# Optimization experiments

Measured on AMD Instinct MI355X. Metric: run time of the kernel, lower is better.

Reference implementation:

```python
import jax, jax.numpy as jnp
import numpy as np

B, T, H, L, OUT = 64, 2048, 256, 2, 256


def setup_inputs() -> dict:
    key = jax.random.key(0)
    ks = jax.random.split(key, 7)
    s = 1.0 / np.sqrt(H)
    return {
        "x": jax.random.normal(ks[0], (B, T, H), dtype=jnp.float32),
        "W_ih": jax.random.uniform(ks[1], (L, 4 * H, H), jnp.float32, -s, s),
        "W_hh": jax.random.uniform(ks[2], (L, 4 * H, H), jnp.float32, -s, s),
        "b_ih": jax.random.uniform(ks[3], (L, 4 * H), jnp.float32, -s, s),
        "b_hh": jax.random.uniform(ks[4], (L, 4 * H), jnp.float32, -s, s),
        "W_fc": jax.random.uniform(ks[5], (OUT, H), jnp.float32, -s, s),
        "b_fc": jax.random.uniform(ks[6], (OUT,), jnp.float32, -s, s),
    }


def _lstm_forward(x, W_ih, W_hh, b_ih, b_hh, W_fc, b_fc):
    n_layers = W_ih.shape[0]
    batch = x.shape[0]
    hidden = W_hh.shape[2]
    h0 = jnp.zeros((n_layers, batch, hidden), x.dtype)
    c0 = jnp.zeros((n_layers, batch, hidden), x.dtype)

    def step(carry, x_t):
        h, c = carry  # [L, B, H] each
        inp = x_t  # [B, in]
        new_h, new_c = [], []
        for l in range(n_layers):
            # gates: [B, 4H] = x W_ih^T + b_ih + h W_hh^T + b_hh
            gates = (inp @ W_ih[l].T + b_ih[l]) + (h[l] @ W_hh[l].T + b_hh[l])
            i_g, f_g, g_g, o_g = jnp.split(gates, 4, axis=-1)
            c_new = jax.nn.sigmoid(f_g) * c[l] + jax.nn.sigmoid(i_g) * jnp.tanh(g_g)
            h_new = jax.nn.sigmoid(o_g) * jnp.tanh(c_new)
            new_h.append(h_new)
            new_c.append(c_new)
            inp = h_new
        return (jnp.stack(new_h), jnp.stack(new_c)), None

    (h_T, _), _ = jax.lax.scan(step, (h0, c0), jnp.swapaxes(x, 0, 1))
    # fc applied to last timestep's top-layer hidden state
    return h_T[-1] @ W_fc.T + b_fc  # [B, OUT]


def reference(x, W_ih, W_hh, b_ih, b_hh, W_fc, b_fc):
    return _lstm_forward(x, W_ih, W_hh, b_ih, b_hh, W_fc, b_fc)
```

## Files before the change

kernel.cpp:

```cpp
#include <hip/hip_runtime.h>
#include <math.h>

typedef unsigned long long u64;
typedef __attribute__((ext_vector_type(8))) short short8v;
typedef __attribute__((ext_vector_type(4))) float f32x4;
typedef __attribute__((ext_vector_type(4))) unsigned uint4v;

#define LB 64
#define LT 2048
#define LH 256
#define LOUT 256
#define NWG 256

#define WS_CNT    0
#define WS_CNT_SZ (12 * 1024)
#define TICK_OFF  2048
#define WS_H1     (64 * 1024)
#define WS_H2     (WS_H1 + 256 * 1024)
#define WS_BIAS   (WS_H2 + 256 * 1024)
#define WS_WT2    (1024 * 1024)

#define MFMA(a, b, c) __builtin_amdgcn_mfma_f32_16x16x32_bf16(a, b, c, 0, 0, 0)

__device__ __host__ __forceinline__ short bf16_rne(float f) {
    unsigned u = __builtin_bit_cast(unsigned, f);
    unsigned r = (u + 0x7fffu + ((u >> 16) & 1u)) >> 16;
    return (short)r;
}
__device__ __forceinline__ float bf16_to_f(short s) {
    unsigned u = ((unsigned)(unsigned short)s) << 16;
    return __builtin_bit_cast(float, u);
}
__device__ __forceinline__ float fsigm(float g) {
    return __builtin_amdgcn_rcpf(1.f + __builtin_amdgcn_exp2f(g * -1.44269504f));
}
__device__ __forceinline__ float ftanh(float g) {
    return __builtin_amdgcn_rcpf(1.f + __builtin_amdgcn_exp2f(g * -2.88539008f)) * 2.f - 1.f;
}

template <int LOCAL>
__device__ __forceinline__ int ld_flag(const int* p) {
    int v; u64 a = (u64)p;
    if (LOCAL) asm volatile("global_load_dword %0, %1, off sc0\n\ts_waitcnt vmcnt(0)"
                            : "=&v"(v) : "v"(a) : "memory");
    else       asm volatile("global_load_dword %0, %1, off sc0 sc1\n\ts_waitcnt vmcnt(0)"
                            : "=&v"(v) : "v"(a) : "memory");
    return v;
}
template <int LOCAL>
__device__ __forceinline__ void st_flag(int* p, int v) {
    u64 a = (u64)p;
    if (LOCAL) asm volatile("global_store_dword %0, %1, off sc0" :: "v"(a), "v"(v) : "memory");
    else       asm volatile("global_store_dword %0, %1, off sc0 sc1" :: "v"(a), "v"(v) : "memory");
}
template <int LOCAL>
__device__ __forceinline__ void st_unit(void* p, uint4v d) {
    u64 a = (u64)p;
    if (LOCAL) asm volatile("global_store_dwordx4 %0, %1, off sc0" :: "v"(a), "v"(d) : "memory");
    else       asm volatile("global_store_dwordx4 %0, %1, off sc0 sc1" :: "v"(a), "v"(d) : "memory");
}
template <int LOCAL>
__device__ __forceinline__ void ld_units(u64 a0, u64 a1, u64 a2, u64 a3,
        uint4v& U0, uint4v& U1, uint4v& U2, uint4v& U3,
        uint4v& U4, uint4v& U5, uint4v& U6, uint4v& U7) {
    if (LOCAL) asm volatile(
        "global_load_dwordx4 %0, %8, off sc0\n\t"
        "global_load_dwordx4 %1, %8, off offset:16 sc0\n\t"
        "global_load_dwordx4 %2, %9, off sc0\n\t"
        "global_load_dwordx4 %3, %9, off offset:16 sc0\n\t"
        "global_load_dwordx4 %4, %10, off sc0\n\t"
        "global_load_dwordx4 %5, %10, off offset:16 sc0\n\t"
        "global_load_dwordx4 %6, %11, off sc0\n\t"
        "global_load_dwordx4 %7, %11, off offset:16 sc0\n\t"
        "s_waitcnt vmcnt(0)"
        : "=&v"(U0), "=&v"(U1), "=&v"(U2), "=&v"(U3),
          "=&v"(U4), "=&v"(U5), "=&v"(U6), "=&v"(U7)
        : "v"(a0), "v"(a1), "v"(a2), "v"(a3) : "memory");
    else asm volatile(
        "global_load_dwordx4 %0, %8, off sc0 sc1\n\t"
        "global_load_dwordx4 %1, %8, off offset:16 sc0 sc1\n\t"
        "global_load_dwordx4 %2, %9, off sc0 sc1\n\t"
        "global_load_dwordx4 %3, %9, off offset:16 sc0 sc1\n\t"
        "global_load_dwordx4 %4, %10, off sc0 sc1\n\t"
        "global_load_dwordx4 %5, %10, off offset:16 sc0 sc1\n\t"
        "global_load_dwordx4 %6, %11, off sc0 sc1\n\t"
        "global_load_dwordx4 %7, %11, off offset:16 sc0 sc1\n\t"
        "s_waitcnt vmcnt(0)"
        : "=&v"(U0), "=&v"(U1), "=&v"(U2), "=&v"(U3),
          "=&v"(U4), "=&v"(U5), "=&v"(U6), "=&v"(U7)
        : "v"(a0), "v"(a1), "v"(a2), "v"(a3) : "memory");
}

__global__ void prep_weights(const float* __restrict__ W_ih,
                             const float* __restrict__ W_hh,
                             const float* __restrict__ b_ih,
                             const float* __restrict__ b_hh,
                             unsigned short* __restrict__ Wt2,
                             float* __restrict__ bias_r) {
    int gid = blockIdx.x * 256 + threadIdx.x;
    if (gid >= (1 << 20)) return;
    int j   = gid & 7;
    int rwi = (gid >> 3) & 15;
    int kgi = (gid >> 7) & 3;
    int ks  = (gid >> 9) & 15;
    int mt  = (gid >> 13) & 3;
    int s   = (gid >> 15) & 15;
    int layer = gid >> 19;
    int k   = ks * 32 + kgi * 8 + j;
    int row = mt * 256 + s * 16 + rwi;
    float w = (k < 256) ? W_ih[((size_t)layer * 1024 + row) * 256 + k]
                        : W_hh[((size_t)layer * 1024 + row) * 256 + (k - 256)];
    short hi = bf16_rne(w);
    float rem = w - bf16_to_f(hi);
    short lo = bf16_rne(rem);
    size_t base = (((size_t)((layer * 16 + s) * 4 + mt) * 16 + ks) * 1024)
                  + (size_t)kgi * 128 + rwi * 8 + j;
    Wt2[base]       = (unsigned short)hi;
    Wt2[base + 512] = (unsigned short)lo;
    if (k == 0) {
        int ridx = s * 64 + mt * 16 + rwi;
        bias_r[layer * 1024 + ridx] = b_ih[layer * 1024 + row] + b_hh[layer * 1024 + row];
    }
}

__global__ __launch_bounds__(256, 1)
void lstm_persistent(const float* __restrict__ x,
                     const unsigned short* __restrict__ Wt2,
                     const float* __restrict__ bias_r,
                     char* __restrict__ h1c, char* __restrict__ h2c,
                     int* __restrict__ cnt)
{
    __shared__ __align__(16) f32x4 red[12][64];
    __shared__ int s_mode, s_bg, s_role;

    const int tid   = threadIdx.x;
    const int wave  = tid >> 6;
    const int lane  = tid & 63;

    if (tid == 0) {
        unsigned xcc = (unsigned)__builtin_amdgcn_s_getreg(20 | (3 << 11)) & 7u;
        int* tick = cnt + TICK_OFF;
        int tk = __hip_atomic_fetch_add(tick + xcc, 1, __ATOMIC_RELAXED, __HIP_MEMORY_SCOPE_AGENT);
        __hip_atomic_fetch_add(tick + 8, 1, __ATOMIC_RELEASE, __HIP_MEMORY_SCOPE_AGENT);
        while (__hip_atomic_load(tick + 8, __ATOMIC_ACQUIRE, __HIP_MEMORY_SCOPE_AGENT) < NWG)
            __builtin_amdgcn_s_sleep(8);
        int bal = 1;
        for (int i = 0; i < 8; ++i)
            bal &= (__hip_atomic_load(tick + i, __ATOMIC_RELAXED, __HIP_MEMORY_SCOPE_AGENT) == 32);
        s_mode = bal;
        s_bg   = bal ? (int)xcc : (int)(blockIdx.x & 7);
        s_role = bal ? tk : (int)(((blockIdx.x >> 7) << 4) | ((blockIdx.x & 127) >> 3));
    }
    __syncthreads();

    __builtin_amdgcn_fence(__ATOMIC_SEQ_CST, "agent");
    __syncthreads();
    if (tid == 0) {
        int* b2 = cnt + TICK_OFF + 16;
        __hip_atomic_fetch_add(b2, 1, __ATOMIC_RELEASE, __HIP_MEMORY_SCOPE_AGENT);
        while (__hip_atomic_load(b2, __ATOMIC_ACQUIRE, __HIP_MEMORY_SCOPE_AGENT) < NWG)
            __builtin_amdgcn_s_sleep(8);
    }
    __syncthreads();

    const int mode  = s_mode;
    const int bg    = s_bg;
    const int layer = s_role >> 4;
    const int s     = s_role & 15;
    const int b0    = bg * 8;
    const int kg    = lane >> 4;
    const int rw    = lane & 15;
    const int rb    = rw & 7;
    const int batch = b0 + rb;
    int* const fl_base = cnt + bg * 256;

    short8v Ahi[4][4], Alo[4][4];
    #pragma unroll
    for (int mt = 0; mt < 4; ++mt)
        #pragma unroll
        for (int k2 = 0; k2 < 4; ++k2) {
            size_t base = (((size_t)((layer * 16 + s) * 4 + mt) * 16 + (wave * 4 + k2)) * 1024)
                          + (size_t)kg * 128 + rw * 8;
            Ahi[mt][k2] = *(const short8v*)((const short*)Wt2 + base);
            Alo[mt][k2] = *(const short8v*)((const short*)Wt2 + base + 512);
        }

    f32x4 biasv[4];
    #pragma unroll
    for (int mt = 0; mt < 4; ++mt)
        biasv[mt] = *(const f32x4*)(bias_r + layer * 1024 + s * 64 + mt * 16 + kg * 4);

    f32x4 creg = {0.f, 0.f, 0.f, 0.f};

    float4 xr[4][2];
    if (layer == 0 && wave < 2) {
        #pragma unroll
        for (int k2 = 0; k2 < 4; ++k2) {
            const int kbase = (wave * 4 + k2) * 32 + kg * 8;
            const float* xp = x + ((size_t)batch * LT + 0) * LH + kbase;
            xr[k2][0] = *(const float4*)xp;
            xr[k2][1] = *(const float4*)(xp + 4);
        }
    }

    for (int r = 0; r <= LT; ++r) {
        const bool active = (layer == 0) ? (r < LT) : (r >= 1);
        const int t = (layer == 0) ? r : (r - 1);

        short8v Bhi[4], Blo[4];
        bool useB = false;
        if (active) {
            if (layer == 0 && wave < 2) {
                #pragma unroll
                for (int k2 = 0; k2 < 4; ++k2) {
                    float fv[8] = {xr[k2][0].x, xr[k2][0].y, xr[k2][0].z, xr[k2][0].w,
                                   xr[k2][1].x, xr[k2][1].y, xr[k2][1].z, xr[k2][1].w};
                    short8v bh, bl;
                    #pragma unroll
                    for (int j = 0; j < 8; ++j) {
                        short hb = bf16_rne(fv[j]);
                        bh[j] = hb;
                        bl[j] = bf16_rne(fv[j] - bf16_to_f(hb));
                    }
                    Bhi[k2] = bh; Blo[k2] = bl;
                }
                useB = true;
            } else {
                const char* hbuf; int slot, kofs; bool any;
                if (layer == 0)      { any = (t > 0); hbuf = h1c; slot = (t - 1) & 3; kofs = -256; }
                else if (wave < 2)   { any = true;    hbuf = h1c; slot = t & 3;       kofs = 0;    }
                else                 { any = (t > 0); hbuf = h2c; slot = (t - 1) & 3; kofs = -256; }
                if (any) {
                    const int kb0 = wave * 128 + kg * 8 + kofs;
                    u64 a0, a1, a2, a3;
                    {
                        int kb;
                        kb = kb0;       a0 = (u64)(hbuf + (size_t)((((slot * 64 + batch) * 16) + (kb >> 4)) * 4 + ((kb >> 2) & 3)) * 16);
                        kb = kb0 + 32;  a1 = (u64)(hbuf + (size_t)((((slot * 64 + batch) * 16) + (kb >> 4)) * 4 + ((kb >> 2) & 3)) * 16);
                        kb = kb0 + 64;  a2 = (u64)(hbuf + (size_t)((((slot * 64 + batch) * 16) + (kb >> 4)) * 4 + ((kb >> 2) & 3)) * 16);
                        kb = kb0 + 96;  a3 = (u64)(hbuf + (size_t)((((slot * 64 + batch) * 16) + (kb >> 4)) * 4 + ((kb >> 2) & 3)) * 16);
                    }
                    uint4v U0, U1, U2, U3, U4, U5, U6, U7;
                    if (mode) ld_units<1>(a0, a1, a2, a3, U0, U1, U2, U3, U4, U5, U6, U7);
                    else      ld_units<0>(a0, a1, a2, a3, U0, U1, U2, U3, U4, U5, U6, U7);
                    union { unsigned d[4]; short8v v; } bh, bl;
                    bh.d[0] = U0.x; bh.d[1] = U0.y; bh.d[2] = U1.x; bh.d[3] = U1.y; Bhi[0] = bh.v;
                    bl.d[0] = U0.z; bl.d[1] = U0.w; bl.d[2] = U1.z; bl.d[3] = U1.w; Blo[0] = bl.v;
                    bh.d[0] = U2.x; bh.d[1] = U2.y; bh.d[2] = U3.x; bh.d[3] = U3.y; Bhi[1] = bh.v;
                    bl.d[0] = U2.z; bl.d[1] = U2.w; bl.d[2] = U3.z; bl.d[3] = U3.w; Blo[1] = bl.v;
                    bh.d[0] = U4.x; bh.d[1] = U4.y; bh.d[2] = U5.x; bh.d[3] = U5.y; Bhi[2] = bh.v;
                    bl.d[0] = U4.z; bl.d[1] = U4.w; bl.d[2] = U5.z; bl.d[3] = U5.w; Blo[2] = bl.v;
                    bh.d[0] = U6.x; bh.d[1] = U6.y; bh.d[2] = U7.x; bh.d[3] = U7.y; Bhi[3] = bh.v;
                    bl.d[0] = U6.z; bl.d[1] = U6.w; bl.d[2] = U7.z; bl.d[3] = U7.w; Blo[3] = bl.v;
                    useB = true;
                }
            }
        }

        f32x4 acc[4];
        #pragma unroll
        for (int mt = 0; mt < 4; ++mt) acc[mt] = (f32x4){0.f, 0.f, 0.f, 0.f};
        if (useB) {
            #pragma unroll
            for (int k2 = 0; k2 < 4; ++k2)
                #pragma unroll
                for (int mt = 0; mt < 4; ++mt) {
                    acc[mt] = MFMA(Ahi[mt][k2], Bhi[k2], acc[mt]);
                    acc[mt] = MFMA(Ahi[mt][k2], Blo[k2], acc[mt]);
                    acc[mt] = MFMA(Alo[mt][k2], Bhi[k2], acc[mt]);
                }
        }

        if (active && wave > 0) {
            #pragma unroll
            for (int mt = 0; mt < 4; ++mt) red[(wave - 1) * 4 + mt][lane] = acc[mt];
        }
        __syncthreads();

        if (active && wave == 0) {
            f32x4 gate[4];
            #pragma unroll
            for (int mt = 0; mt < 4; ++mt) {
                f32x4 gs = acc[mt] + biasv[mt];
                #pragma unroll
                for (int w = 0; w < 3; ++w) gs += red[w * 4 + mt][lane];
                gate[mt] = gs;
            }
            float hv[4];
            #pragma unroll
            for (int rr = 0; rr < 4; ++rr) {
                float si = fsigm(gate[0][rr]);
                float sf = fsigm(gate[1][rr]);
                float so = fsigm(gate[3][rr]);
                float gg = ftanh(gate[2][rr]);
                float cn = sf * creg[rr] + si * gg;
                creg[rr] = cn;
                hv[rr] = so * ftanh(cn);
            }
            if (rw < 8) {
                u64 qh = 0, ql = 0;
                #pragma unroll
                for (int rr = 0; rr < 4; ++rr) {
                    unsigned short hb = (unsigned short)bf16_rne(hv[rr]);
                    unsigned short lb = (unsigned short)bf16_rne(hv[rr] - bf16_to_f((short)hb));
                    qh |= ((u64)hb) << (16 * rr);
                    ql |= ((u64)lb) << (16 * rr);
                }
                uint4v dd;
                dd.x = (unsigned)qh; dd.y = (unsigned)(qh >> 32);
                dd.z = (unsigned)ql; dd.w = (unsigned)(ql >> 32);
                char* hbuf = (layer == 0 ? h1c : h2c);
                int unit = (((t & 3) * 64 + (b0 + rw)) * 16 + s) * 4 + kg;
                if (mode) st_unit<1>(hbuf + (size_t)unit * 16, dd);
                else      st_unit<0>(hbuf + (size_t)unit * 16, dd);
            }
        }

        if (wave == 0 && r < LT) {
            asm volatile("s_waitcnt vmcnt(0)" ::: "memory");
            if (lane == 0) {
                int* fp = fl_base + (layer * 16 + s) * 16;
                if (mode) { st_flag<1>(fp, r + 1); st_flag<0>(fp, r + 1); }
                else      st_flag<0>(fp, r + 1);
            }
        }

        if (layer == 0 && wave < 2 && t + 1 < LT) {
            #pragma unroll
            for (int k2 = 0; k2 < 4; ++k2) {
                const int kbase = (wave * 4 + k2) * 32 + kg * 8;
                const float* xp = x + ((size_t)batch * LT + (t + 1)) * LH + kbase;
                xr[k2][0] = *(const float4*)xp;
                xr[k2][1] = *(const float4*)(xp + 4);
            }
        }

        if (r < LT) {
            if (wave == 0) {
                const int mL  = lane >> 4;
                const int tgt = (layer == 0) ? ((mL == 0) ? r + 1 : r - 1) : (r + 1);
                int* fp = fl_base + (lane & 31) * 16;
                int it = 0;
                for (;;) {
                    int v = 0x7fffffff;
                    if (lane < 32) {
                        ++it;
                        if (mode && (it & 7) != 0) v = ld_flag<1>(fp);
                        else                       v = ld_flag<0>(fp);
                    }
                    if (__all(v >= tgt)) break;
                    if (!mode) __builtin_amdgcn_s_sleep(1);
                }
            }
            __syncthreads();
        }
    }
}

__global__ __launch_bounds__(256)
void fc_kernel(const char* __restrict__ h2c,
               const float* __restrict__ W_fc,
               const float* __restrict__ b_fc,
               float* __restrict__ out) {
    int b = blockIdx.x;
    int o = threadIdx.x;
    __shared__ float hrow[LH];
    for (int k = threadIdx.x; k < LH; k += 256) {
        int unit = ((3 * 64 + b) * 16 + (k >> 4)) * 4 + ((k >> 2) & 3);
        const u64* up = (const u64*)(h2c + (size_t)unit * 16);
        u64 qh = up[0];
        u64 ql = up[1];
        int sh = (k & 3) * 16;
        hrow[k] = bf16_to_f((short)(qh >> sh)) + bf16_to_f((short)(ql >> sh));
    }
    __syncthreads();
    float acc = b_fc[o];
#pragma unroll 8
    for (int k = 0; k < LH; ++k)
        acc = fmaf(W_fc[o * LH + k], hrow[k], acc);
    out[b * LOUT + o] = acc;
}

extern "C" void kernel_launch(void* const* d_in, const int* in_sizes, int n_in,
                              void* d_out, int out_size, void* d_ws, size_t ws_size,
                              hipStream_t stream) {
    const float* x    = (const float*)d_in[0];
    const float* W_ih = (const float*)d_in[1];
    const float* W_hh = (const float*)d_in[2];
    const float* b_ih = (const float*)d_in[3];
    const float* b_hh = (const float*)d_in[4];
    const float* W_fc = (const float*)d_in[5];
    const float* b_fc = (const float*)d_in[6];
    float* out = (float*)d_out;

    char* ws = (char*)d_ws;
    int*            cnt    = (int*)(ws + WS_CNT);
    char*           h1c    = ws + WS_H1;
    char*           h2c    = ws + WS_H2;
    float*          bias_r = (float*)(ws + WS_BIAS);
    unsigned short* Wt2    = (unsigned short*)(ws + WS_WT2);

    hipMemsetAsync(cnt, 0, WS_CNT_SZ, stream);
    prep_weights<<<(1 << 20) / 256, 256, 0, stream>>>(W_ih, W_hh, b_ih, b_hh, Wt2, bias_r);

    void* args[] = {(void*)&x, (void*)&Wt2, (void*)&bias_r,
                    (void*)&h1c, (void*)&h2c, (void*)&cnt};
    hipError_t e = hipLaunchCooperativeKernel(lstm_persistent, dim3(NWG), dim3(256),
                                              args, 0, stream);
    if (e != hipSuccess) {
        lstm_persistent<<<NWG, 256, 0, stream>>>(x, Wt2, bias_r, h1c, h2c, cnt);
    }

    fc_kernel<<<LB, 256, 0, stream>>>(h2c, W_fc, b_fc, out);
}
```

Before: 8.370 ms.

## Distribute LSTM gate epilogue across all four waves with per-wave dword stores

Instead of wave 0 reducing partial gate sums from the other three waves and computing all four batch-row cell updates, every wave now writes its partials to shared memory and computes one cell element (selected by wave index), storing a packed hi/lo bf16 dword. The hidden-state layout changes from hi/lo 64-bit halves to interleaved hi/lo per element, so the consumer unpack and the fc kernel are adjusted to match. The x prefetch is moved before the MFMA section, and the flag publish moves after a new barrier, dropping the duplicate local store and polling the slower coherent path less often. This aims to shorten the serial epilogue on the critical path of each timestep, at the cost of an extra __syncthreads and four times as many narrower global stores per unit.

```diff
diff --git a/kernel.cpp b/kernel.cpp
--- a/kernel.cpp
+++ b/kernel.cpp
@@ -54,10 +54,10 @@
     else       asm volatile("global_store_dword %0, %1, off sc0 sc1" :: "v"(a), "v"(v) : "memory");
 }
 template <int LOCAL>
-__device__ __forceinline__ void st_unit(void* p, uint4v d) {
+__device__ __forceinline__ void st_dw(void* p, unsigned d) {
     u64 a = (u64)p;
-    if (LOCAL) asm volatile("global_store_dwordx4 %0, %1, off sc0" :: "v"(a), "v"(d) : "memory");
-    else       asm volatile("global_store_dwordx4 %0, %1, off sc0 sc1" :: "v"(a), "v"(d) : "memory");
+    if (LOCAL) asm volatile("global_store_dword %0, %1, off sc0" :: "v"(a), "v"(d) : "memory");
+    else       asm volatile("global_store_dword %0, %1, off sc0 sc1" :: "v"(a), "v"(d) : "memory");
 }
 template <int LOCAL>
 __device__ __forceinline__ void ld_units(u64 a0, u64 a1, u64 a2, u64 a3,
@@ -91,6 +91,21 @@
         : "v"(a0), "v"(a1), "v"(a2), "v"(a3) : "memory");
 }
 
+__device__ __forceinline__ void unpack_frag(const uint4v& Ua, const uint4v& Ub,
+                                            short8v& bh, short8v& bl) {
+    union { unsigned d[4]; short8v v; } H, L;
+    H.d[0] = (Ua.x & 0xffffu) | (Ua.y << 16);
+    H.d[1] = (Ua.z & 0xffffu) | (Ua.w << 16);
+    H.d[2] = (Ub.x & 0xffffu) | (Ub.y << 16);
+    H.d[3] = (Ub.z & 0xffffu) | (Ub.w << 16);
+    L.d[0] = (Ua.x >> 16) | (Ua.y & 0xffff0000u);
+    L.d[1] = (Ua.z >> 16) | (Ua.w & 0xffff0000u);
+    L.d[2] = (Ub.x >> 16) | (Ub.w & 0xffff0000u & 0xffff0000u) ;
+    L.d[2] = (Ub.x >> 16) | (Ub.y & 0xffff0000u);
+    L.d[3] = (Ub.z >> 16) | (Ub.w & 0xffff0000u);
+    bh = H.v; bl = L.v;
+}
+
 __global__ void prep_weights(const float* __restrict__ W_ih,
                              const float* __restrict__ W_hh,
                              const float* __restrict__ b_ih,
@@ -130,7 +145,7 @@
                      char* __restrict__ h1c, char* __restrict__ h2c,
                      int* __restrict__ cnt)
 {
-    __shared__ __align__(16) f32x4 red[12][64];
+    __shared__ __align__(16) f32x4 red[16][64];
     __shared__ int s_mode, s_bg, s_role;
 
     const int tid   = threadIdx.x;
@@ -185,12 +200,12 @@
             Alo[mt][k2] = *(const short8v*)((const short*)Wt2 + base + 512);
         }
 
-    f32x4 biasv[4];
+    float bias_w[4];
     #pragma unroll
     for (int mt = 0; mt < 4; ++mt)
-        biasv[mt] = *(const f32x4*)(bias_r + layer * 1024 + s * 64 + mt * 16 + kg * 4);
-
-    f32x4 creg = {0.f, 0.f, 0.f, 0.f};
+        bias_w[mt] = bias_r[layer * 1024 + s * 64 + mt * 16 + kg * 4 + wave];
+
+    float creg = 0.f;
 
     float4 xr[4][2];
     if (layer == 0 && wave < 2) {
@@ -225,6 +240,15 @@
                     Bhi[k2] = bh; Blo[k2] = bl;
                 }
                 useB = true;
+                if (t + 1 < LT) {
+                    #pragma unroll
+                    for (int k2 = 0; k2 < 4; ++k2) {
+                        const int kbase = (wave * 4 + k2) * 32 + kg * 8;
+                        const float* xp = x + ((size_t)batch * LT + (t + 1)) * LH + kbase;
+                        xr[k2][0] = *(const float4*)xp;
+                        xr[k2][1] = *(const float4*)(xp + 4);
+                    }
+                }
             } else {
                 const char* hbuf; int slot, kofs; bool any;
                 if (layer == 0)      { any = (t > 0); hbuf = h1c; slot = (t - 1) & 3; kofs = -256; }
@@ -243,15 +267,10 @@
                     uint4v U0, U1, U2, U3, U4, U5, U6, U7;
                     if (mode) ld_units<1>(a0, a1, a2, a3, U0, U1, U2, U3, U4, U5, U6, U7);
                     else      ld_units<0>(a0, a1, a2, a3, U0, U1, U2, U3, U4, U5, U6, U7);
-                    union { unsigned d[4]; short8v v; } bh, bl;
-                    bh.d[0] = U0.x; bh.d[1] = U0.y; bh.d[2] = U1.x; bh.d[3] = U1.y; Bhi[0] = bh.v;
-                    bl.d[0] = U0.z; bl.d[1] = U0.w; bl.d[2] = U1.z; bl.d[3] = U1.w; Blo[0] = bl.v;
-                    bh.d[0] = U2.x; bh.d[1] = U2.y; bh.d[2] = U3.x; bh.d[3] = U3.y; Bhi[1] = bh.v;
-                    bl.d[0] = U2.z; bl.d[1] = U2.w; bl.d[2] = U3.z; bl.d[3] = U3.w; Blo[1] = bl.v;
-                    bh.d[0] = U4.x; bh.d[1] = U4.y; bh.d[2] = U5.x; bh.d[3] = U5.y; Bhi[2] = bh.v;
-                    bl.d[0] = U4.z; bl.d[1] = U4.w; bl.d[2] = U5.z; bl.d[3] = U5.w; Blo[2] = bl.v;
-                    bh.d[0] = U6.x; bh.d[1] = U6.y; bh.d[2] = U7.x; bh.d[3] = U7.y; Bhi[3] = bh.v;
-                    bl.d[0] = U6.z; bl.d[1] = U6.w; bl.d[2] = U7.z; bl.d[3] = U7.w; Blo[3] = bl.v;
+                    unpack_frag(U0, U1, Bhi[0], Blo[0]);
+                    unpack_frag(U2, U3, Bhi[1], Blo[1]);
+                    unpack_frag(U4, U5, Bhi[2], Blo[2]);
+                    unpack_frag(U6, U7, Bhi[3], Blo[3]);
                     useB = true;
                 }
             }
@@ -271,72 +290,50 @@
                 }
         }
 
-        if (active && wave > 0) {
+        if (active) {
             #pragma unroll
-            for (int mt = 0; mt < 4; ++mt) red[(wave - 1) * 4 + mt][lane] = acc[mt];
+            for (int mt = 0; mt < 4; ++mt) red[wave * 4 + mt][lane] = acc[mt];
         }
         __syncthreads();
 
-        if (active && wave == 0) {
-            f32x4 gate[4];
+        if (active) {
+            float g[4];
             #pragma unroll
             for (int mt = 0; mt < 4; ++mt) {
-                f32x4 gs = acc[mt] + biasv[mt];
+                float sum = bias_w[mt];
                 #pragma unroll
-                for (int w = 0; w < 3; ++w) gs += red[w * 4 + mt][lane];
-                gate[mt] = gs;
+                for (int src = 0; src < 4; ++src) {
+                    const float* rp = (const float*)&red[src * 4 + mt][lane];
+                    sum += rp[wave];
+                }
+                g[mt] = sum;
             }
-            float hv[4];
-            #pragma unroll
-            for (int rr = 0; rr < 4; ++rr) {
-                float si = fsigm(gate[0][rr]);
-                float sf = fsigm(gate[1][rr]);
-                float so = fsigm(gate[3][rr]);
-                float gg = ftanh(gate[2][rr]);
-                float cn = sf * creg[rr] + si * gg;
-                creg[rr] = cn;
-                hv[rr] = so * ftanh(cn);
-            }
+            float si = fsigm(g[0]);
+            float sf = fsigm(g[1]);
+            float so = fsigm(g[3]);
+            float gg = ftanh(g[2]);
+            float cn = sf * creg + si * gg;
+            creg = cn;
+            float hn = so * ftanh(cn);
             if (rw < 8) {
-                u64 qh = 0, ql = 0;
-                #pragma unroll
-                for (int rr = 0; rr < 4; ++rr) {
-                    unsigned short hb = (unsigned short)bf16_rne(hv[rr]);
-                    unsigned short lb = (unsigned short)bf16_rne(hv[rr] - bf16_to_f((short)hb));
-                    qh |= ((u64)hb) << (16 * rr);
-                    ql |= ((u64)lb) << (16 * rr);
-                }
-                uint4v dd;
-                dd.x = (unsigned)qh; dd.y = (unsigned)(qh >> 32);
-                dd.z = (unsigned)ql; dd.w = (unsigned)(ql >> 32);
+                unsigned short hb = (unsigned short)bf16_rne(hn);
+                unsigned short lb = (unsigned short)bf16_rne(hn - bf16_to_f((short)hb));
+                unsigned d = (unsigned)hb | ((unsigned)lb << 16);
                 char* hbuf = (layer == 0 ? h1c : h2c);
                 int unit = (((t & 3) * 64 + (b0 + rw)) * 16 + s) * 4 + kg;
-                if (mode) st_unit<1>(hbuf + (size_t)unit * 16, dd);
-                else      st_unit<0>(hbuf + (size_t)unit * 16, dd);
+                void* ad = hbuf + (size_t)unit * 16 + wave * 4;
+                if (mode) st_dw<1>(ad, d); else st_dw<0>(ad, d);
             }
         }
-
-        if (wave == 0 && r < LT) {
-            asm volatile("s_waitcnt vmcnt(0)" ::: "memory");
-            if (lane == 0) {
-                int* fp = fl_base + (layer * 16 + s) * 16;
-                if (mode) { st_flag<1>(fp, r + 1); st_flag<0>(fp, r + 1); }
-                else      st_flag<0>(fp, r + 1);
-            }
-        }
-
-        if (layer == 0 && wave < 2 && t + 1 < LT) {
-            #pragma unroll
-            for (int k2 = 0; k2 < 4; ++k2) {
-                const int kbase = (wave * 4 + k2) * 32 + kg * 8;
-                const float* xp = x + ((size_t)batch * LT + (t + 1)) * LH + kbase;
-                xr[k2][0] = *(const float4*)xp;
-                xr[k2][1] = *(const float4*)(xp + 4);
-            }
-        }
+        __syncthreads();
 
         if (r < LT) {
             if (wave == 0) {
+                if (lane == 0) {
+                    int* fp = fl_base + (layer * 16 + s) * 16;
+                    if (mode) st_flag<1>(fp, r + 1);
+                    else      st_flag<0>(fp, r + 1);
+                }
                 const int mL  = lane >> 4;
                 const int tgt = (layer == 0) ? ((mL == 0) ? r + 1 : r - 1) : (r + 1);
                 int* fp = fl_base + (lane & 31) * 16;
@@ -345,8 +342,8 @@
                     int v = 0x7fffffff;
                     if (lane < 32) {
                         ++it;
-                        if (mode && (it & 7) != 0) v = ld_flag<1>(fp);
-                        else                       v = ld_flag<0>(fp);
+                        if (mode && (it & 63) != 0) v = ld_flag<1>(fp);
+                        else                        v = ld_flag<0>(fp);
                     }
                     if (__all(v >= tgt)) break;
                     if (!mode) __builtin_amdgcn_s_sleep(1);
@@ -367,11 +364,8 @@
     __shared__ float hrow[LH];
     for (int k = threadIdx.x; k < LH; k += 256) {
         int unit = ((3 * 64 + b) * 16 + (k >> 4)) * 4 + ((k >> 2) & 3);
-        const u64* up = (const u64*)(h2c + (size_t)unit * 16);
-        u64 qh = up[0];
-        u64 ql = up[1];
-        int sh = (k & 3) * 16;
-        hrow[k] = bf16_to_f((short)(qh >> sh)) + bf16_to_f((short)(ql >> sh));
+        unsigned d = ((const unsigned*)(h2c + (size_t)unit * 16))[k & 3];
+        hrow[k] = bf16_to_f((short)(d & 0xffff)) + bf16_to_f((short)(d >> 16));
     }
     __syncthreads();
     float acc = b_fc[o];
```

After: 21.41 ms. 2.56x slower.
